# Kernel optimization log

Hardware: AMD Instinct MI355X
Metric: run time of the kernel (lower is better)

The kernel has to match this reference:

```python
import jax, jax.numpy as jnp
import numpy as np

B, K, L, H = 64, 32, 64, 256


def setup_inputs() -> dict:
    key = jax.random.key(0)
    ks = jax.random.split(key, 24)
    def rnd(i, shape, scale):
        return jax.random.normal(ks[i], shape, dtype=jnp.float32) * scale
    s = 0.05  # small init for weights to keep activations sane
    return {
        'h_ue': rnd(0, (B, K, H), 1.0),
        'h_ap': rnd(1, (B, L, H), 1.0),
        'e':    rnd(2, (B, L * K, H), 1.0),
        # msg_ap_to_ue: Linear(2H->H), Linear(H->H)
        'a2u_w1': rnd(3, (H, 2 * H), s), 'a2u_b1': rnd(4, (H,), s),
        'a2u_w2': rnd(5, (H, H), s),     'a2u_b2': rnd(6, (H,), s),
        # msg_ue_to_ap
        'u2a_w1': rnd(7, (H, 2 * H), s), 'u2a_b1': rnd(8, (H,), s),
        'u2a_w2': rnd(9, (H, H), s),     'u2a_b2': rnd(10, (H,), s),
        # GRUCell (PyTorch layout: weight_ih (3H,H), weight_hh (3H,H))
        'ue_wih': rnd(11, (3 * H, H), s), 'ue_bih': rnd(12, (3 * H,), s),
        'ue_whh': rnd(13, (3 * H, H), s), 'ue_bhh': rnd(14, (3 * H,), s),
        'ap_wih': rnd(15, (3 * H, H), s), 'ap_bih': rnd(16, (3 * H,), s),
        'ap_whh': rnd(17, (3 * H, H), s), 'ap_bhh': rnd(18, (3 * H,), s),
        # edge_update: Linear(3H->H), Linear(H->H)
        'ed_w1': rnd(19, (H, 3 * H), s), 'ed_b1': rnd(20, (H,), s),
        'ed_w2': rnd(21, (H, H), s),     'ed_b2': rnd(22, (H,), s),
    }


def _gru(x, h, wih, bih, whh, bhh):
    # PyTorch GRUCell semantics
    gi = jnp.einsum('...h,oh->...o', x, wih) + bih
    gh = jnp.einsum('...h,oh->...o', h, whh) + bhh
    i_r, i_z, i_n = jnp.split(gi, 3, axis=-1)
    h_r, h_z, h_n = jnp.split(gh, 3, axis=-1)
    r = jax.nn.sigmoid(i_r + h_r)
    z = jax.nn.sigmoid(i_z + h_z)
    n = jnp.tanh(i_n + r * h_n)
    return (1.0 - z) * n + z * h


def reference(h_ue, h_ap, e,
              a2u_w1, a2u_b1, a2u_w2, a2u_b2,
              u2a_w1, u2a_b1, u2a_w2, u2a_b2,
              ue_wih, ue_bih, ue_whh, ue_bhh,
              ap_wih, ap_bih, ap_whh, ap_bhh,
              ed_w1, ed_b1, ed_w2, ed_b2):
    Bd, Kd, Hd = h_ue.shape
    Ld = h_ap.shape[1]
    e4 = e.reshape(Bd, Ld, Kd, Hd)  # edge (b, l, k) on dense bipartite graph

    # --- AP -> UE messages: MLP(concat[h_ap_src, e]); split first linear ---
    pre = (jnp.einsum('blh,oh->blo', h_ap, a2u_w1[:, :Hd])[:, :, None, :]
           + jnp.einsum('blkh,oh->blko', e4, a2u_w1[:, Hd:]) + a2u_b1)
    msg = jnp.einsum('blkh,oh->blko', jax.nn.relu(pre), a2u_w2) + a2u_b2
    m_ue = msg.mean(axis=1)  # mean over AP neighbors -> (B,K,H)

    # --- UE -> AP messages ---
    pre = (jnp.einsum('bkh,oh->bko', h_ue, u2a_w1[:, :Hd])[:, None, :, :]
           + jnp.einsum('blkh,oh->blko', e4, u2a_w1[:, Hd:]) + u2a_b1)
    msg = jnp.einsum('blkh,oh->blko', jax.nn.relu(pre), u2a_w2) + u2a_b2
    m_ap = msg.mean(axis=2)  # mean over UE neighbors -> (B,L,H)

    # --- GRU node updates ---
    h_ue_new = _gru(m_ue, h_ue, ue_wih, ue_bih, ue_whh, ue_bhh)
    h_ap_new = _gru(m_ap, h_ap, ap_wih, ap_bih, ap_whh, ap_bhh)

    # --- edge update: MLP(concat[src=UE_new, dst=AP_new, e]) ---
    pre = (jnp.einsum('bkh,oh->bko', h_ue_new, ed_w1[:, :Hd])[:, None, :, :]
           + jnp.einsum('blh,oh->blo', h_ap_new, ed_w1[:, Hd:2 * Hd])[:, :, None, :]
           + jnp.einsum('blkh,oh->blko', e4, ed_w1[:, 2 * Hd:]) + ed_b1)
    e_new = jnp.einsum('blkh,oh->blko', jax.nn.relu(pre), ed_w2) + ed_b2

    return h_ue_new, h_ap_new, e_new.reshape(Bd, Ld * Kd, Hd)
```

## Files before the change

### kernel.cpp

```cpp
#include <hip/hip_runtime.h>

#define HH 256
#define BB 64
#define KK 32
#define LL 64
#define LGRP 8

typedef __bf16 bf16_t;
typedef __attribute__((ext_vector_type(8))) __bf16 bf16x8;
typedef __attribute__((ext_vector_type(4))) float f32x4;

__device__ __forceinline__ bf16x8 ld_a8(const float* __restrict__ p) {
  const f32x4* q = (const f32x4*)p;
  f32x4 a = q[0], b = q[1];
  bf16x8 r;
  r[0] = (__bf16)a[0]; r[1] = (__bf16)a[1]; r[2] = (__bf16)a[2]; r[3] = (__bf16)a[3];
  r[4] = (__bf16)b[0]; r[5] = (__bf16)b[1]; r[6] = (__bf16)b[2]; r[7] = (__bf16)b[3];
  return r;
}

__device__ __forceinline__ void ld_tile(const float* __restrict__ E, int tid, f32x4 r[4]) {
  const f32x4* q = (const f32x4*)(E + tid * 16);
  r[0] = q[0]; r[1] = q[1]; r[2] = q[2]; r[3] = q[3];
}
__device__ __forceinline__ void wr_tile(bf16_t* buf, int tid, const f32x4 r[4]) {
  int row = tid >> 4;
  int colb = (tid & 15) * 32;
  bf16x8 v0, v1;
  v0[0] = (__bf16)r[0][0]; v0[1] = (__bf16)r[0][1]; v0[2] = (__bf16)r[0][2]; v0[3] = (__bf16)r[0][3];
  v0[4] = (__bf16)r[1][0]; v0[5] = (__bf16)r[1][1]; v0[6] = (__bf16)r[1][2]; v0[7] = (__bf16)r[1][3];
  v1[0] = (__bf16)r[2][0]; v1[1] = (__bf16)r[2][1]; v1[2] = (__bf16)r[2][2]; v1[3] = (__bf16)r[2][3];
  v1[4] = (__bf16)r[3][0]; v1[5] = (__bf16)r[3][1]; v1[6] = (__bf16)r[3][2]; v1[7] = (__bf16)r[3][3];
  int swz = (row & 7) << 4;
  *(bf16x8*)((char*)buf + row * 512 + (colb ^ swz)) = v0;
  *(bf16x8*)((char*)buf + row * 512 + ((colb + 16) ^ swz)) = v1;
}

template<int LDB>
__device__ __forceinline__ void mm_f32A(const float* __restrict__ A,
                                        const bf16_t* __restrict__ B,
                                        f32x4 acc[2][4], int lane) {
  const int c = lane & 15, g = lane >> 4;
#pragma unroll
  for (int ks = 0; ks < 8; ++ks) {
    const int ko = ks * 32 + g * 8;
    bf16x8 a0 = ld_a8(A + c * HH + ko);
    bf16x8 a1 = ld_a8(A + (16 + c) * HH + ko);
#pragma unroll
    for (int nt = 0; nt < 4; ++nt) {
      bf16x8 bb = *(const bf16x8*)(B + (nt * 16 + c) * LDB + ko);
      acc[0][nt] = __builtin_amdgcn_mfma_f32_16x16x32_bf16(a0, bb, acc[0][nt], 0, 0, 0);
      acc[1][nt] = __builtin_amdgcn_mfma_f32_16x16x32_bf16(a1, bb, acc[1][nt], 0, 0, 0);
    }
  }
}

__global__ __launch_bounds__(256) void prep_kernel(
    const float* w0, const float* w1, const float* w2, const float* w3,
    const float* w4, const float* w5, const float* w6, const float* w7,
    const float* w8, const float* w9, bf16_t* wb) {
  int i = blockIdx.x * 256 + threadIdx.x;
  const float* s; int o; float sc = 1.f;
  if      (i < 131072)  { s = w0; o = i; }
  else if (i < 196608)  { s = w1; o = i - 131072; sc = 1.f / 64.f; }
  else if (i < 327680)  { s = w2; o = i - 196608; }
  else if (i < 393216)  { s = w3; o = i - 327680; sc = 1.f / 32.f; }
  else if (i < 589824)  { s = w4; o = i - 393216; }
  else if (i < 786432)  { s = w5; o = i - 589824; }
  else if (i < 983040)  { s = w6; o = i - 786432; }
  else if (i < 1179648) { s = w7; o = i - 983040; }
  else if (i < 1376256) { s = w8; o = i - 1179648; }
  else                  { s = w9; o = i - 1376256; }
  wb[i] = (__bf16)(s[o] * sc);
}

template<int LDW>
__global__ __launch_bounds__(256) void proj2_kernel(
    const float* __restrict__ X0, const bf16_t* __restrict__ W0,
    const float* __restrict__ b0, float* __restrict__ out0, int n0,
    const float* __restrict__ X1, const bf16_t* __restrict__ W1,
    const float* __restrict__ b1, float* __restrict__ out1) {
  const int blk = blockIdx.x;
  const float* X; const bf16_t* W; const float* bias; float* out; int row0;
  if (blk < n0) { X = X0; W = W0; bias = b0; out = out0; row0 = blk * 32; }
  else          { X = X1; W = W1; bias = b1; out = out1; row0 = (blk - n0) * 32; }
  const int tid = threadIdx.x, w = tid >> 6, lane = tid & 63;
  const int colw = w * 64, c = lane & 15, g = lane >> 4;
  f32x4 acc[2][4];
#pragma unroll
  for (int nt = 0; nt < 4; ++nt) {
    float bv = bias ? bias[colw + nt * 16 + c] : 0.f;
    f32x4 t = {bv, bv, bv, bv};
    acc[0][nt] = t; acc[1][nt] = t;
  }
  mm_f32A<LDW>(X + (size_t)row0 * HH, W + (size_t)colw * LDW, acc, lane);
#pragma unroll
  for (int m = 0; m < 2; ++m)
#pragma unroll
    for (int nt = 0; nt < 4; ++nt)
#pragma unroll
      for (int rr = 0; rr < 4; ++rr) {
        int row = row0 + m * 16 + g * 4 + rr;
        out[(size_t)row * HH + colw + nt * 16 + c] = acc[m][nt][rr];
      }
}

__global__ __launch_bounds__(512) void phaseA_kernel(
    const float* __restrict__ e, const float* __restrict__ p_ap,
    const float* __restrict__ p_ue,
    const bf16_t* __restrict__ wu1e, const bf16_t* __restrict__ wa1e,
    float* __restrict__ part, float* __restrict__ R_ap) {
  __shared__ bf16_t ebuf[2][32 * 256];
  const int blk = blockIdx.x;
  const int b = blk >> 3, lc = blk & 7;
  const int tid = threadIdx.x, w = tid >> 6, lane = tid & 63;
  const int colw = w * 32, c = lane & 15, g = lane >> 4;
  const int l0 = lc * LGRP;

  bf16x8 wU[2][8], wA[2][8];
#pragma unroll
  for (int nt = 0; nt < 2; ++nt)
#pragma unroll
    for (int ks = 0; ks < 8; ++ks) {
      size_t off = (size_t)(colw + nt * 16 + c) * 512 + ks * 32 + g * 8;
      wU[nt][ks] = *(const bf16x8*)(wu1e + off);
      wA[nt][ks] = *(const bf16x8*)(wa1e + off);
    }

  float pue[2][2][4];
#pragma unroll
  for (int m = 0; m < 2; ++m)
#pragma unroll
    for (int nt = 0; nt < 2; ++nt)
#pragma unroll
      for (int rr = 0; rr < 4; ++rr)
        pue[m][nt][rr] = p_ue[(size_t)(b * KK + m * 16 + g * 4 + rr) * HH + colw + nt * 16 + c];

  f32x4 accU[2][2];
  const f32x4 z4 = {0.f, 0.f, 0.f, 0.f};
#pragma unroll
  for (int m = 0; m < 2; ++m)
#pragma unroll
    for (int nt = 0; nt < 2; ++nt) accU[m][nt] = z4;

  f32x4 rs[4];
  ld_tile(e + (size_t)((b * LL + l0) * KK) * HH, tid, rs);
  wr_tile(ebuf[0], tid, rs);

  for (int li = 0; li < LGRP; ++li) {
    __syncthreads();
    const int l = l0 + li;
    if (li + 1 < LGRP) ld_tile(e + (size_t)((b * LL + l + 1) * KK) * HH, tid, rs);

    f32x4 aU[2][2], aA[2][2];
#pragma unroll
    for (int nt = 0; nt < 2; ++nt) {
      float pa = p_ap[(size_t)(b * LL + l) * HH + colw + nt * 16 + c];
      f32x4 t = {pa, pa, pa, pa};
      aA[0][nt] = t; aA[1][nt] = t;
#pragma unroll
      for (int rr = 0; rr < 4; ++rr) {
        aU[0][nt][rr] = pue[0][nt][rr];
        aU[1][nt][rr] = pue[1][nt][rr];
      }
    }
    const bf16_t* eb = ebuf[li & 1];
    const int swz = (c & 7) << 4;
#pragma unroll
    for (int ks = 0; ks < 8; ++ks) {
      const int kb = (ks * 32 + g * 8) * 2;
      bf16x8 a0 = *(const bf16x8*)((const char*)eb + c * 512 + (kb ^ swz));
      bf16x8 a1 = *(const bf16x8*)((const char*)eb + (16 + c) * 512 + (kb ^ swz));
#pragma unroll
      for (int nt = 0; nt < 2; ++nt) {
        aU[0][nt] = __builtin_amdgcn_mfma_f32_16x16x32_bf16(a0, wU[nt][ks], aU[0][nt], 0, 0, 0);
        aU[1][nt] = __builtin_amdgcn_mfma_f32_16x16x32_bf16(a1, wU[nt][ks], aU[1][nt], 0, 0, 0);
        aA[0][nt] = __builtin_amdgcn_mfma_f32_16x16x32_bf16(a0, wA[nt][ks], aA[0][nt], 0, 0, 0);
        aA[1][nt] = __builtin_amdgcn_mfma_f32_16x16x32_bf16(a1, wA[nt][ks], aA[1][nt], 0, 0, 0);
      }
    }
    __syncthreads();
    if (li + 1 < LGRP) wr_tile(ebuf[(li + 1) & 1], tid, rs);

#pragma unroll
    for (int nt = 0; nt < 2; ++nt) {
      float s = 0.f;
#pragma unroll
      for (int m = 0; m < 2; ++m)
#pragma unroll
        for (int rr = 0; rr < 4; ++rr) s += fmaxf(aU[m][nt][rr], 0.f);
      s += __shfl_xor(s, 16);
      s += __shfl_xor(s, 32);
      if (lane < 16)
        R_ap[(size_t)(b * LL + l) * HH + colw + nt * 16 + lane] = s;
    }
#pragma unroll
    for (int m = 0; m < 2; ++m)
#pragma unroll
      for (int nt = 0; nt < 2; ++nt)
#pragma unroll
        for (int rr = 0; rr < 4; ++rr)
          accU[m][nt][rr] += fmaxf(aA[m][nt][rr], 0.f);
  }

#pragma unroll
  for (int m = 0; m < 2; ++m)
#pragma unroll
    for (int nt = 0; nt < 2; ++nt)
#pragma unroll
      for (int rr = 0; rr < 4; ++rr) {
        int krow = m * 16 + g * 4 + rr;
        part[(size_t)((lc * BB + b) * KK + krow) * HH + colw + nt * 16 + c] = accU[m][nt][rr];
      }
}

__global__ __launch_bounds__(256) void reduce_kernel(
    const float* __restrict__ part, float* __restrict__ R_ue) {
  int i = blockIdx.x * 256 + threadIdx.x;
  float s = 0.f;
#pragma unroll
  for (int lc = 0; lc < 8; ++lc) s += part[(size_t)lc * 524288 + i];
  R_ue[i] = s;
}

__global__ __launch_bounds__(256) void gru_kernel(
    const float* __restrict__ m_ue, const float* __restrict__ h_ue,
    const bf16_t* __restrict__ wih_ue, const bf16_t* __restrict__ whh_ue,
    const float* __restrict__ ue_bih, const float* __restrict__ ue_bhh,
    float* __restrict__ hue_new,
    const float* __restrict__ m_ap, const float* __restrict__ h_ap,
    const bf16_t* __restrict__ wih_ap, const bf16_t* __restrict__ whh_ap,
    const float* __restrict__ ap_bih, const float* __restrict__ ap_bhh,
    float* __restrict__ hap_new) {
  const int blk = blockIdx.x;
  const float *x, *h, *bih, *bhh; const bf16_t *wih, *whh; float* hout; int row0;
  if (blk < 64) { x = m_ue; h = h_ue; wih = wih_ue; whh = whh_ue;
                  bih = ue_bih; bhh = ue_bhh; hout = hue_new; row0 = blk * 32; }
  else          { x = m_ap; h = h_ap; wih = wih_ap; whh = whh_ap;
                  bih = ap_bih; bhh = ap_bhh; hout = hap_new; row0 = (blk - 64) * 32; }
  const int tid = threadIdx.x, w = tid >> 6, lane = tid & 63;
  const int colw = w * 64, c = lane & 15, g = lane >> 4;
  f32x4 aR[2][4], aZ[2][4], aN[2][4], aHN[2][4];
#pragma unroll
  for (int nt = 0; nt < 4; ++nt) {
    int col = colw + nt * 16 + c;
    float vR = bih[col] + bhh[col];
    float vZ = bih[256 + col] + bhh[256 + col];
    float vN = bih[512 + col];
    float vH = bhh[512 + col];
    f32x4 tR = {vR, vR, vR, vR}, tZ = {vZ, vZ, vZ, vZ};
    f32x4 tN = {vN, vN, vN, vN}, tH = {vH, vH, vH, vH};
    aR[0][nt] = tR; aR[1][nt] = tR;
    aZ[0][nt] = tZ; aZ[1][nt] = tZ;
    aN[0][nt] = tN; aN[1][nt] = tN;
    aHN[0][nt] = tH; aHN[1][nt] = tH;
  }
  const float* X = x + (size_t)row0 * HH;
  const float* Hp = h + (size_t)row0 * HH;
  mm_f32A<256>(X,  wih + (size_t)(0   + colw) * 256, aR, lane);
  mm_f32A<256>(Hp, whh + (size_t)(0   + colw) * 256, aR, lane);
  mm_f32A<256>(X,  wih + (size_t)(256 + colw) * 256, aZ, lane);
  mm_f32A<256>(Hp, whh + (size_t)(256 + colw) * 256, aZ, lane);
  mm_f32A<256>(X,  wih + (size_t)(512 + colw) * 256, aN, lane);
  mm_f32A<256>(Hp, whh + (size_t)(512 + colw) * 256, aHN, lane);
#pragma unroll
  for (int m = 0; m < 2; ++m)
#pragma unroll
    for (int nt = 0; nt < 4; ++nt)
#pragma unroll
      for (int rr = 0; rr < 4; ++rr) {
        int row = row0 + m * 16 + g * 4 + rr;
        int col = colw + nt * 16 + c;
        float rg = 1.f / (1.f + __expf(-aR[m][nt][rr]));
        float zg = 1.f / (1.f + __expf(-aZ[m][nt][rr]));
        float t = aN[m][nt][rr] + rg * aHN[m][nt][rr];
        t = fminf(fmaxf(t, -15.f), 15.f);
        float ex = __expf(-2.f * t);
        float ng = (1.f - ex) / (1.f + ex);
        float ho = h[(size_t)row * HH + col];
        hout[(size_t)row * HH + col] = (1.f - zg) * ng + zg * ho;
      }
}

__global__ __launch_bounds__(512) void phaseC_kernel(
    const float* __restrict__ e, const float* __restrict__ q_ue,
    const float* __restrict__ q_ap,
    const bf16_t* __restrict__ wed1e, const bf16_t* __restrict__ wed2,
    const float* __restrict__ ed_b2, float* __restrict__ e_new) {
  __shared__ bf16_t ebuf[2][32 * 256];
  __shared__ bf16_t pbuf[32 * 256];
  const int blk = blockIdx.x;
  const int b = blk >> 3, lc = blk & 7;
  const int tid = threadIdx.x, w = tid >> 6, lane = tid & 63;
  const int colw = w * 32, c = lane & 15, g = lane >> 4;
  const int l0 = lc * LGRP;

  bf16x8 w1[2][8], w2[2][8];
#pragma unroll
  for (int nt = 0; nt < 2; ++nt)
#pragma unroll
    for (int ks = 0; ks < 8; ++ks) {
      w1[nt][ks] = *(const bf16x8*)(wed1e + (size_t)(colw + nt * 16 + c) * 768 + ks * 32 + g * 8);
      w2[nt][ks] = *(const bf16x8*)(wed2  + (size_t)(colw + nt * 16 + c) * 256 + ks * 32 + g * 8);
    }

  float qU[2][2][4];
#pragma unroll
  for (int m = 0; m < 2; ++m)
#pragma unroll
    for (int nt = 0; nt < 2; ++nt)
#pragma unroll
      for (int rr = 0; rr < 4; ++rr)
        qU[m][nt][rr] = q_ue[(size_t)(b * KK + m * 16 + g * 4 + rr) * HH + colw + nt * 16 + c];
  float b2v[2];
#pragma unroll
  for (int nt = 0; nt < 2; ++nt) b2v[nt] = ed_b2[colw + nt * 16 + c];

  f32x4 rs[4];
  ld_tile(e + (size_t)((b * LL + l0) * KK) * HH, tid, rs);
  wr_tile(ebuf[0], tid, rs);

  for (int li = 0; li < LGRP; ++li) {
    __syncthreads();
    const int l = l0 + li;

    f32x4 a1[2][2];
#pragma unroll
    for (int nt = 0; nt < 2; ++nt) {
      float qa = q_ap[(size_t)(b * LL + l) * HH + colw + nt * 16 + c];
#pragma unroll
      for (int rr = 0; rr < 4; ++rr) {
        a1[0][nt][rr] = qa + qU[0][nt][rr];
        a1[1][nt][rr] = qa + qU[1][nt][rr];
      }
    }
    const bf16_t* eb = ebuf[li & 1];
    const int swz = (c & 7) << 4;
#pragma unroll
    for (int ks = 0; ks < 8; ++ks) {
      const int kb = (ks * 32 + g * 8) * 2;
      bf16x8 a0 = *(const bf16x8*)((const char*)eb + c * 512 + (kb ^ swz));
      bf16x8 a1f = *(const bf16x8*)((const char*)eb + (16 + c) * 512 + (kb ^ swz));
#pragma unroll
      for (int nt = 0; nt < 2; ++nt) {
        a1[0][nt] = __builtin_amdgcn_mfma_f32_16x16x32_bf16(a0,  w1[nt][ks], a1[0][nt], 0, 0, 0);
        a1[1][nt] = __builtin_amdgcn_mfma_f32_16x16x32_bf16(a1f, w1[nt][ks], a1[1][nt], 0, 0, 0);
      }
    }
    if (li + 1 < LGRP) ld_tile(e + (size_t)((b * LL + l + 1) * KK) * HH, tid, rs);

#pragma unroll
    for (int m = 0; m < 2; ++m)
#pragma unroll
      for (int nt = 0; nt < 2; ++nt)
#pragma unroll
        for (int rr = 0; rr < 4; ++rr) {
          int row = m * 16 + g * 4 + rr;
          int col = colw + nt * 16 + c;
          float v = fmaxf(a1[m][nt][rr], 0.f);
          int off = row * 512 + ((col * 2) ^ ((row & 7) << 4));
          *(bf16_t*)((char*)pbuf + off) = (__bf16)v;
        }
    __syncthreads();

    f32x4 a2[2][2];
#pragma unroll
    for (int nt = 0; nt < 2; ++nt) {
      f32x4 t = {b2v[nt], b2v[nt], b2v[nt], b2v[nt]};
      a2[0][nt] = t; a2[1][nt] = t;
    }
#pragma unroll
    for (int ks = 0; ks < 8; ++ks) {
      const int kb = (ks * 32 + g * 8) * 2;
      bf16x8 a0 = *(const bf16x8*)((const char*)pbuf + c * 512 + (kb ^ swz));
      bf16x8 a1f = *(const bf16x8*)((const char*)pbuf + (16 + c) * 512 + (kb ^ swz));
#pragma unroll
      for (int nt = 0; nt < 2; ++nt) {
        a2[0][nt] = __builtin_amdgcn_mfma_f32_16x16x32_bf16(a0,  w2[nt][ks], a2[0][nt], 0, 0, 0);
        a2[1][nt] = __builtin_amdgcn_mfma_f32_16x16x32_bf16(a1f, w2[nt][ks], a2[1][nt], 0, 0, 0);
      }
    }
#pragma unroll
    for (int m = 0; m < 2; ++m)
#pragma unroll
      for (int nt = 0; nt < 2; ++nt)
#pragma unroll
        for (int rr = 0; rr < 4; ++rr) {
          int row = m * 16 + g * 4 + rr;
          e_new[(size_t)((b * LL + l) * KK + row) * HH + colw + nt * 16 + c] = a2[m][nt][rr];
        }
    if (li + 1 < LGRP) wr_tile(ebuf[(li + 1) & 1], tid, rs);
  }
}

extern "C" void kernel_launch(void* const* d_in, const int* in_sizes, int n_in,
                              void* d_out, int out_size, void* d_ws, size_t ws_size,
                              hipStream_t stream) {
  const float* h_ue   = (const float*)d_in[0];
  const float* h_ap   = (const float*)d_in[1];
  const float* e      = (const float*)d_in[2];
  const float* a2u_w1 = (const float*)d_in[3];
  const float* a2u_b1 = (const float*)d_in[4];
  const float* a2u_w2 = (const float*)d_in[5];
  const float* a2u_b2 = (const float*)d_in[6];
  const float* u2a_w1 = (const float*)d_in[7];
  const float* u2a_b1 = (const float*)d_in[8];
  const float* u2a_w2 = (const float*)d_in[9];
  const float* u2a_b2 = (const float*)d_in[10];
  const float* ue_wih = (const float*)d_in[11];
  const float* ue_bih = (const float*)d_in[12];
  const float* ue_whh = (const float*)d_in[13];
  const float* ue_bhh = (const float*)d_in[14];
  const float* ap_wih = (const float*)d_in[15];
  const float* ap_bih = (const float*)d_in[16];
  const float* ap_whh = (const float*)d_in[17];
  const float* ap_bhh = (const float*)d_in[18];
  const float* ed_w1  = (const float*)d_in[19];
  const float* ed_b1  = (const float*)d_in[20];
  const float* ed_w2  = (const float*)d_in[21];
  const float* ed_b2  = (const float*)d_in[22];

  bf16_t* wb      = (bf16_t*)d_ws;
  bf16_t* wa1     = wb;
  bf16_t* wa2s    = wa1 + 131072;
  bf16_t* wu1     = wa2s + 65536;
  bf16_t* wu2s    = wu1 + 131072;
  bf16_t* wih_ue  = wu2s + 65536;
  bf16_t* whh_ue  = wih_ue + 196608;
  bf16_t* wih_ap  = whh_ue + 196608;
  bf16_t* whh_ap  = wih_ap + 196608;
  bf16_t* wed1    = whh_ap + 196608;
  bf16_t* wed2    = wed1 + 196608;
  float* fbase = (float*)((char*)d_ws + 2883584);
  float* m_ue = fbase;
  float* m_ap = m_ue + 524288;
  float* p_ap = m_ap + 1048576;
  float* p_ue = p_ap + 1048576;
  float* q_ue = p_ue + 524288;
  float* q_ap = q_ue + 524288;
  float* part = q_ap + 1048576;
  float* R_ue = q_ue;
  float* R_ap = q_ap;

  float* out      = (float*)d_out;
  float* hue_new  = out;
  float* hap_new  = out + 524288;
  float* e_new    = out + 1572864;

  prep_kernel<<<5632, 256, 0, stream>>>(a2u_w1, a2u_w2, u2a_w1, u2a_w2,
                                        ue_wih, ue_whh, ap_wih, ap_whh,
                                        ed_w1, ed_w2, wb);
  proj2_kernel<512><<<192, 256, 0, stream>>>(h_ap, wa1, a2u_b1, p_ap, 128,
                                             h_ue, wu1, u2a_b1, p_ue);
  phaseA_kernel<<<512, 512, 0, stream>>>(e, p_ap, p_ue, wu1 + 256, wa1 + 256,
                                         part, R_ap);
  reduce_kernel<<<2048, 256, 0, stream>>>(part, R_ue);
  proj2_kernel<256><<<192, 256, 0, stream>>>(R_ue, wa2s, a2u_b2, m_ue, 64,
                                             R_ap, wu2s, u2a_b2, m_ap);
  gru_kernel<<<192, 256, 0, stream>>>(m_ue, h_ue, wih_ue, whh_ue, ue_bih, ue_bhh, hue_new,
                                      m_ap, h_ap, wih_ap, whh_ap, ap_bih, ap_bhh, hap_new);
  proj2_kernel<768><<<192, 256, 0, stream>>>(hue_new, wed1, ed_b1, q_ue, 64,
                                             hap_new, wed1 + 256, nullptr, q_ap);
  phaseC_kernel<<<512, 512, 0, stream>>>(e, q_ue, q_ap, wed1 + 512, wed2, ed_b2, e_new);
}
```

Measured before the change: 221.8 us.

## Fuse prep, projection, reduce and GRU kernels into three launches

Drops the weight-prep kernel and the separate projection, reduce and GRU launches. Weights are converted from fp32 to bf16 on the fly inside the consumers. The node projections are now computed redundantly inside phaseA and phaseC per block, and node_kernel fuses the partial-sum reduction, message linear and GRU, staging the message in LDS. This cuts launches from eight to three and removes intermediate buffers, at the cost of redundant per-block projection work and repeated fp32 weight loads and conversions.

Result: slower. 337.5 us (+52.1%).

```diff
diff --git a/kernel.cpp b/kernel.cpp
--- a/kernel.cpp
+++ b/kernel.cpp
@@ -16,6 +16,26 @@
   bf16x8 r;
   r[0] = (__bf16)a[0]; r[1] = (__bf16)a[1]; r[2] = (__bf16)a[2]; r[3] = (__bf16)a[3];
   r[4] = (__bf16)b[0]; r[5] = (__bf16)b[1]; r[6] = (__bf16)b[2]; r[7] = (__bf16)b[3];
+  return r;
+}
+__device__ __forceinline__ bf16x8 ld_a8s(const float* __restrict__ p, float sc) {
+  const f32x4* q = (const f32x4*)p;
+  f32x4 a = q[0], b = q[1];
+  bf16x8 r;
+  r[0] = (__bf16)(a[0]*sc); r[1] = (__bf16)(a[1]*sc); r[2] = (__bf16)(a[2]*sc); r[3] = (__bf16)(a[3]*sc);
+  r[4] = (__bf16)(b[0]*sc); r[5] = (__bf16)(b[1]*sc); r[6] = (__bf16)(b[2]*sc); r[7] = (__bf16)(b[3]*sc);
+  return r;
+}
+__device__ __forceinline__ bf16x8 ld_sum8(const float* __restrict__ p) {
+  f32x4 s0 = {0.f,0.f,0.f,0.f}, s1 = s0;
+#pragma unroll
+  for (int lc = 0; lc < 8; ++lc) {
+    const f32x4* q = (const f32x4*)(p + (size_t)lc * 524288);
+    s0 += q[0]; s1 += q[1];
+  }
+  bf16x8 r;
+  r[0] = (__bf16)s0[0]; r[1] = (__bf16)s0[1]; r[2] = (__bf16)s0[2]; r[3] = (__bf16)s0[3];
+  r[4] = (__bf16)s1[0]; r[5] = (__bf16)s1[1]; r[6] = (__bf16)s1[2]; r[7] = (__bf16)s1[3];
   return r;
 }
 
@@ -37,104 +57,146 @@
 }
 
 template<int LDB>
-__device__ __forceinline__ void mm_f32A(const float* __restrict__ A,
-                                        const bf16_t* __restrict__ B,
-                                        f32x4 acc[2][4], int lane) {
+__device__ __forceinline__ void mm_f32AB(const float* __restrict__ A,
+                                         const float* __restrict__ B,
+                                         f32x4 acc[2][4], int lane, float sc) {
   const int c = lane & 15, g = lane >> 4;
 #pragma unroll
   for (int ks = 0; ks < 8; ++ks) {
     const int ko = ks * 32 + g * 8;
-    bf16x8 a0 = ld_a8(A + c * HH + ko);
-    bf16x8 a1 = ld_a8(A + (16 + c) * HH + ko);
+    bf16x8 a0 = ld_a8(A + (size_t)c * HH + ko);
+    bf16x8 a1 = ld_a8(A + (size_t)(16 + c) * HH + ko);
 #pragma unroll
     for (int nt = 0; nt < 4; ++nt) {
-      bf16x8 bb = *(const bf16x8*)(B + (nt * 16 + c) * LDB + ko);
+      bf16x8 bb = ld_a8s(B + (size_t)(nt * 16 + c) * LDB + ko, sc);
       acc[0][nt] = __builtin_amdgcn_mfma_f32_16x16x32_bf16(a0, bb, acc[0][nt], 0, 0, 0);
       acc[1][nt] = __builtin_amdgcn_mfma_f32_16x16x32_bf16(a1, bb, acc[1][nt], 0, 0, 0);
     }
   }
 }
 
-__global__ __launch_bounds__(256) void prep_kernel(
-    const float* w0, const float* w1, const float* w2, const float* w3,
-    const float* w4, const float* w5, const float* w6, const float* w7,
-    const float* w8, const float* w9, bf16_t* wb) {
-  int i = blockIdx.x * 256 + threadIdx.x;
-  const float* s; int o; float sc = 1.f;
-  if      (i < 131072)  { s = w0; o = i; }
-  else if (i < 196608)  { s = w1; o = i - 131072; sc = 1.f / 64.f; }
-  else if (i < 327680)  { s = w2; o = i - 196608; }
-  else if (i < 393216)  { s = w3; o = i - 327680; sc = 1.f / 32.f; }
-  else if (i < 589824)  { s = w4; o = i - 393216; }
-  else if (i < 786432)  { s = w5; o = i - 589824; }
-  else if (i < 983040)  { s = w6; o = i - 786432; }
-  else if (i < 1179648) { s = w7; o = i - 983040; }
-  else if (i < 1376256) { s = w8; o = i - 1179648; }
-  else                  { s = w9; o = i - 1376256; }
-  wb[i] = (__bf16)(s[o] * sc);
-}
-
-template<int LDW>
-__global__ __launch_bounds__(256) void proj2_kernel(
-    const float* __restrict__ X0, const bf16_t* __restrict__ W0,
-    const float* __restrict__ b0, float* __restrict__ out0, int n0,
-    const float* __restrict__ X1, const bf16_t* __restrict__ W1,
-    const float* __restrict__ b1, float* __restrict__ out1) {
-  const int blk = blockIdx.x;
-  const float* X; const bf16_t* W; const float* bias; float* out; int row0;
-  if (blk < n0) { X = X0; W = W0; bias = b0; out = out0; row0 = blk * 32; }
-  else          { X = X1; W = W1; bias = b1; out = out1; row0 = (blk - n0) * 32; }
-  const int tid = threadIdx.x, w = tid >> 6, lane = tid & 63;
-  const int colw = w * 64, c = lane & 15, g = lane >> 4;
-  f32x4 acc[2][4];
-#pragma unroll
-  for (int nt = 0; nt < 4; ++nt) {
-    float bv = bias ? bias[colw + nt * 16 + c] : 0.f;
-    f32x4 t = {bv, bv, bv, bv};
-    acc[0][nt] = t; acc[1][nt] = t;
-  }
-  mm_f32A<LDW>(X + (size_t)row0 * HH, W + (size_t)colw * LDW, acc, lane);
-#pragma unroll
-  for (int m = 0; m < 2; ++m)
-#pragma unroll
-    for (int nt = 0; nt < 4; ++nt)
-#pragma unroll
-      for (int rr = 0; rr < 4; ++rr) {
-        int row = row0 + m * 16 + g * 4 + rr;
-        out[(size_t)row * HH + colw + nt * 16 + c] = acc[m][nt][rr];
-      }
+__device__ __forceinline__ void mm_partA(const float* __restrict__ P,
+                                         const float* __restrict__ B,
+                                         f32x4 acc[2][4], int lane, float sc) {
+  const int c = lane & 15, g = lane >> 4;
+#pragma unroll
+  for (int ks = 0; ks < 8; ++ks) {
+    const int ko = ks * 32 + g * 8;
+    bf16x8 a0 = ld_sum8(P + (size_t)c * HH + ko);
+    bf16x8 a1 = ld_sum8(P + (size_t)(16 + c) * HH + ko);
+#pragma unroll
+    for (int nt = 0; nt < 4; ++nt) {
+      bf16x8 bb = ld_a8s(B + (size_t)(nt * 16 + c) * HH + ko, sc);
+      acc[0][nt] = __builtin_amdgcn_mfma_f32_16x16x32_bf16(a0, bb, acc[0][nt], 0, 0, 0);
+      acc[1][nt] = __builtin_amdgcn_mfma_f32_16x16x32_bf16(a1, bb, acc[1][nt], 0, 0, 0);
+    }
+  }
+}
+
+__device__ __forceinline__ void mm_lds_f32B(const bf16_t* lds,
+                                            const float* __restrict__ B,
+                                            f32x4 acc[2][4], int lane) {
+  const int c = lane & 15, g = lane >> 4;
+  const int swz = (c & 7) << 4;
+#pragma unroll
+  for (int ks = 0; ks < 8; ++ks) {
+    const int kb = (ks * 32 + g * 8) * 2;
+    bf16x8 a0 = *(const bf16x8*)((const char*)lds + c * 512 + (kb ^ swz));
+    bf16x8 a1 = *(const bf16x8*)((const char*)lds + (16 + c) * 512 + (kb ^ swz));
+#pragma unroll
+    for (int nt = 0; nt < 4; ++nt) {
+      bf16x8 bb = ld_a8(B + (size_t)(nt * 16 + c) * HH + ks * 32 + g * 8);
+      acc[0][nt] = __builtin_amdgcn_mfma_f32_16x16x32_bf16(a0, bb, acc[0][nt], 0, 0, 0);
+      acc[1][nt] = __builtin_amdgcn_mfma_f32_16x16x32_bf16(a1, bb, acc[1][nt], 0, 0, 0);
+    }
+  }
 }
 
 __global__ __launch_bounds__(512) void phaseA_kernel(
-    const float* __restrict__ e, const float* __restrict__ p_ap,
-    const float* __restrict__ p_ue,
-    const bf16_t* __restrict__ wu1e, const bf16_t* __restrict__ wa1e,
+    const float* __restrict__ e, const float* __restrict__ h_ue,
+    const float* __restrict__ h_ap,
+    const float* __restrict__ a2u_w1, const float* __restrict__ a2u_b1,
+    const float* __restrict__ u2a_w1, const float* __restrict__ u2a_b1,
     float* __restrict__ part, float* __restrict__ R_ap) {
   __shared__ bf16_t ebuf[2][32 * 256];
+  __shared__ float pA[8 * 256];
   const int blk = blockIdx.x;
   const int b = blk >> 3, lc = blk & 7;
   const int tid = threadIdx.x, w = tid >> 6, lane = tid & 63;
   const int colw = w * 32, c = lane & 15, g = lane >> 4;
   const int l0 = lc * LGRP;
 
+  f32x4 rs[4];
+  ld_tile(e + (size_t)((b * LL + l0) * KK) * HH, tid, rs);
+
+  float pue[2][2][4];
+  {
+    f32x4 pacc[2][2];
+#pragma unroll
+    for (int nt = 0; nt < 2; ++nt) {
+      float bv = u2a_b1[colw + nt * 16 + c];
+      f32x4 t = {bv, bv, bv, bv};
+      pacc[0][nt] = t; pacc[1][nt] = t;
+    }
+#pragma unroll
+    for (int ks = 0; ks < 8; ++ks) {
+      const int ko = ks * 32 + g * 8;
+      bf16x8 a0 = ld_a8(h_ue + (size_t)(b * KK + c) * HH + ko);
+      bf16x8 a1 = ld_a8(h_ue + (size_t)(b * KK + 16 + c) * HH + ko);
+#pragma unroll
+      for (int nt = 0; nt < 2; ++nt) {
+        bf16x8 bb = ld_a8(u2a_w1 + (size_t)(colw + nt * 16 + c) * 512 + ko);
+        pacc[0][nt] = __builtin_amdgcn_mfma_f32_16x16x32_bf16(a0, bb, pacc[0][nt], 0, 0, 0);
+        pacc[1][nt] = __builtin_amdgcn_mfma_f32_16x16x32_bf16(a1, bb, pacc[1][nt], 0, 0, 0);
+      }
+    }
+#pragma unroll
+    for (int m = 0; m < 2; ++m)
+#pragma unroll
+      for (int nt = 0; nt < 2; ++nt)
+#pragma unroll
+        for (int rr = 0; rr < 4; ++rr) pue[m][nt][rr] = pacc[m][nt][rr];
+  }
+
+  {
+    f32x4 sap[2];
+#pragma unroll
+    for (int nt = 0; nt < 2; ++nt) {
+      float bv = a2u_b1[colw + nt * 16 + c];
+      f32x4 t = {bv, bv, bv, bv};
+      sap[nt] = t;
+    }
+    const float* Xap = h_ap + (size_t)(b * LL + l0) * HH;
+#pragma unroll
+    for (int ks = 0; ks < 8; ++ks) {
+      const int ko = ks * 32 + g * 8;
+      bf16x8 a = ld_a8(Xap + (size_t)(c & 7) * HH + ko);
+#pragma unroll
+      for (int nt = 0; nt < 2; ++nt) {
+        bf16x8 bb = ld_a8(a2u_w1 + (size_t)(colw + nt * 16 + c) * 512 + ko);
+        sap[nt] = __builtin_amdgcn_mfma_f32_16x16x32_bf16(a, bb, sap[nt], 0, 0, 0);
+      }
+    }
+    if (g < 2) {
+#pragma unroll
+      for (int nt = 0; nt < 2; ++nt)
+#pragma unroll
+        for (int rr = 0; rr < 4; ++rr)
+          pA[(g * 4 + rr) * 256 + colw + nt * 16 + c] = sap[nt][rr];
+    }
+  }
+
   bf16x8 wU[2][8], wA[2][8];
 #pragma unroll
   for (int nt = 0; nt < 2; ++nt)
 #pragma unroll
     for (int ks = 0; ks < 8; ++ks) {
-      size_t off = (size_t)(colw + nt * 16 + c) * 512 + ks * 32 + g * 8;
-      wU[nt][ks] = *(const bf16x8*)(wu1e + off);
-      wA[nt][ks] = *(const bf16x8*)(wa1e + off);
-    }
-
-  float pue[2][2][4];
-#pragma unroll
-  for (int m = 0; m < 2; ++m)
-#pragma unroll
-    for (int nt = 0; nt < 2; ++nt)
-#pragma unroll
-      for (int rr = 0; rr < 4; ++rr)
-        pue[m][nt][rr] = p_ue[(size_t)(b * KK + m * 16 + g * 4 + rr) * HH + colw + nt * 16 + c];
+      size_t off = (size_t)(colw + nt * 16 + c) * 512 + 256 + ks * 32 + g * 8;
+      wU[nt][ks] = ld_a8(u2a_w1 + off);
+      wA[nt][ks] = ld_a8(a2u_w1 + off);
+    }
+
+  wr_tile(ebuf[0], tid, rs);
 
   f32x4 accU[2][2];
   const f32x4 z4 = {0.f, 0.f, 0.f, 0.f};
@@ -142,10 +204,6 @@
   for (int m = 0; m < 2; ++m)
 #pragma unroll
     for (int nt = 0; nt < 2; ++nt) accU[m][nt] = z4;
-
-  f32x4 rs[4];
-  ld_tile(e + (size_t)((b * LL + l0) * KK) * HH, tid, rs);
-  wr_tile(ebuf[0], tid, rs);
 
   for (int li = 0; li < LGRP; ++li) {
     __syncthreads();
@@ -155,7 +213,7 @@
     f32x4 aU[2][2], aA[2][2];
 #pragma unroll
     for (int nt = 0; nt < 2; ++nt) {
-      float pa = p_ap[(size_t)(b * LL + l) * HH + colw + nt * 16 + c];
+      float pa = pA[li * 256 + colw + nt * 16 + c];
       f32x4 t = {pa, pa, pa, pa};
       aA[0][nt] = t; aA[1][nt] = t;
 #pragma unroll
@@ -214,32 +272,56 @@
       }
 }
 
-__global__ __launch_bounds__(256) void reduce_kernel(
-    const float* __restrict__ part, float* __restrict__ R_ue) {
-  int i = blockIdx.x * 256 + threadIdx.x;
-  float s = 0.f;
-#pragma unroll
-  for (int lc = 0; lc < 8; ++lc) s += part[(size_t)lc * 524288 + i];
-  R_ue[i] = s;
-}
-
-__global__ __launch_bounds__(256) void gru_kernel(
-    const float* __restrict__ m_ue, const float* __restrict__ h_ue,
-    const bf16_t* __restrict__ wih_ue, const bf16_t* __restrict__ whh_ue,
-    const float* __restrict__ ue_bih, const float* __restrict__ ue_bhh,
-    float* __restrict__ hue_new,
-    const float* __restrict__ m_ap, const float* __restrict__ h_ap,
-    const bf16_t* __restrict__ wih_ap, const bf16_t* __restrict__ whh_ap,
-    const float* __restrict__ ap_bih, const float* __restrict__ ap_bhh,
-    float* __restrict__ hap_new) {
+__global__ __launch_bounds__(256) void node_kernel(
+    const float* __restrict__ part, const float* __restrict__ R_ap,
+    const float* __restrict__ a2u_w2, const float* __restrict__ a2u_b2,
+    const float* __restrict__ u2a_w2, const float* __restrict__ u2a_b2,
+    const float* __restrict__ h_ue, const float* __restrict__ ue_wih,
+    const float* __restrict__ ue_bih, const float* __restrict__ ue_whh,
+    const float* __restrict__ ue_bhh,
+    const float* __restrict__ h_ap, const float* __restrict__ ap_wih,
+    const float* __restrict__ ap_bih, const float* __restrict__ ap_whh,
+    const float* __restrict__ ap_bhh,
+    float* __restrict__ hue_new, float* __restrict__ hap_new) {
+  __shared__ bf16_t mbuf[32 * 256];
   const int blk = blockIdx.x;
-  const float *x, *h, *bih, *bhh; const bf16_t *wih, *whh; float* hout; int row0;
-  if (blk < 64) { x = m_ue; h = h_ue; wih = wih_ue; whh = whh_ue;
-                  bih = ue_bih; bhh = ue_bhh; hout = hue_new; row0 = blk * 32; }
-  else          { x = m_ap; h = h_ap; wih = wih_ap; whh = whh_ap;
-                  bih = ap_bih; bhh = ap_bhh; hout = hap_new; row0 = (blk - 64) * 32; }
+  const bool ue = blk < 64;
+  const int row0 = ue ? blk * 32 : (blk - 64) * 32;
   const int tid = threadIdx.x, w = tid >> 6, lane = tid & 63;
   const int colw = w * 64, c = lane & 15, g = lane >> 4;
+  const float* W2  = ue ? a2u_w2 : u2a_w2;
+  const float* b2  = ue ? a2u_b2 : u2a_b2;
+  const float* h   = ue ? h_ue : h_ap;
+  const float* wih = ue ? ue_wih : ap_wih;
+  const float* whh = ue ? ue_whh : ap_whh;
+  const float* bih = ue ? ue_bih : ap_bih;
+  const float* bhh = ue ? ue_bhh : ap_bhh;
+  float* hout      = ue ? hue_new : hap_new;
+  const float sc   = ue ? (1.f / 64.f) : (1.f / 32.f);
+
+  f32x4 acc[2][4];
+#pragma unroll
+  for (int nt = 0; nt < 4; ++nt) {
+    float bv = b2[colw + nt * 16 + c];
+    f32x4 t = {bv, bv, bv, bv};
+    acc[0][nt] = t; acc[1][nt] = t;
+  }
+  if (ue) mm_partA(part + (size_t)row0 * HH, W2 + (size_t)colw * HH, acc, lane, sc);
+  else    mm_f32AB<HH>(R_ap + (size_t)row0 * HH, W2 + (size_t)colw * HH, acc, lane, sc);
+
+#pragma unroll
+  for (int m = 0; m < 2; ++m)
+#pragma unroll
+    for (int nt = 0; nt < 4; ++nt)
+#pragma unroll
+      for (int rr = 0; rr < 4; ++rr) {
+        int row = m * 16 + g * 4 + rr;
+        int col = colw + nt * 16 + c;
+        int off = row * 512 + ((col * 2) ^ ((row & 7) << 4));
+        *(bf16_t*)((char*)mbuf + off) = (__bf16)acc[m][nt][rr];
+      }
+  __syncthreads();
+
   f32x4 aR[2][4], aZ[2][4], aN[2][4], aHN[2][4];
 #pragma unroll
   for (int nt = 0; nt < 4; ++nt) {
@@ -255,14 +337,13 @@
     aN[0][nt] = tN; aN[1][nt] = tN;
     aHN[0][nt] = tH; aHN[1][nt] = tH;
   }
-  const float* X = x + (size_t)row0 * HH;
   const float* Hp = h + (size_t)row0 * HH;
-  mm_f32A<256>(X,  wih + (size_t)(0   + colw) * 256, aR, lane);
-  mm_f32A<256>(Hp, whh + (size_t)(0   + colw) * 256, aR, lane);
-  mm_f32A<256>(X,  wih + (size_t)(256 + colw) * 256, aZ, lane);
-  mm_f32A<256>(Hp, whh + (size_t)(256 + colw) * 256, aZ, lane);
-  mm_f32A<256>(X,  wih + (size_t)(512 + colw) * 256, aN, lane);
-  mm_f32A<256>(Hp, whh + (size_t)(512 + colw) * 256, aHN, lane);
+  mm_lds_f32B(mbuf, wih + (size_t)(0   + colw) * HH, aR, lane);
+  mm_f32AB<HH>(Hp,  whh + (size_t)(0   + colw) * HH, aR, lane, 1.f);
+  mm_lds_f32B(mbuf, wih + (size_t)(256 + colw) * HH, aZ, lane);
+  mm_f32AB<HH>(Hp,  whh + (size_t)(256 + colw) * HH, aZ, lane, 1.f);
+  mm_lds_f32B(mbuf, wih + (size_t)(512 + colw) * HH, aN, lane);
+  mm_f32AB<HH>(Hp,  whh + (size_t)(512 + colw) * HH, aHN, lane, 1.f);
 #pragma unroll
   for (int m = 0; m < 2; ++m)
 #pragma unroll
@@ -283,41 +364,88 @@
 }
 
 __global__ __launch_bounds__(512) void phaseC_kernel(
-    const float* __restrict__ e, const float* __restrict__ q_ue,
-    const float* __restrict__ q_ap,
-    const bf16_t* __restrict__ wed1e, const bf16_t* __restrict__ wed2,
-    const float* __restrict__ ed_b2, float* __restrict__ e_new) {
+    const float* __restrict__ e, const float* __restrict__ hue_new,
+    const float* __restrict__ hap_new,
+    const float* __restrict__ ed_w1, const float* __restrict__ ed_b1,
+    const float* __restrict__ ed_w2, const float* __restrict__ ed_b2,
+    float* __restrict__ e_new) {
   __shared__ bf16_t ebuf[2][32 * 256];
   __shared__ bf16_t pbuf[32 * 256];
+  __shared__ float qA[8 * 256];
   const int blk = blockIdx.x;
   const int b = blk >> 3, lc = blk & 7;
   const int tid = threadIdx.x, w = tid >> 6, lane = tid & 63;
   const int colw = w * 32, c = lane & 15, g = lane >> 4;
   const int l0 = lc * LGRP;
 
-  bf16x8 w1[2][8], w2[2][8];
-#pragma unroll
-  for (int nt = 0; nt < 2; ++nt)
-#pragma unroll
-    for (int ks = 0; ks < 8; ++ks) {
-      w1[nt][ks] = *(const bf16x8*)(wed1e + (size_t)(colw + nt * 16 + c) * 768 + ks * 32 + g * 8);
-      w2[nt][ks] = *(const bf16x8*)(wed2  + (size_t)(colw + nt * 16 + c) * 256 + ks * 32 + g * 8);
-    }
-
-  float qU[2][2][4];
-#pragma unroll
-  for (int m = 0; m < 2; ++m)
-#pragma unroll
-    for (int nt = 0; nt < 2; ++nt)
-#pragma unroll
-      for (int rr = 0; rr < 4; ++rr)
-        qU[m][nt][rr] = q_ue[(size_t)(b * KK + m * 16 + g * 4 + rr) * HH + colw + nt * 16 + c];
-  float b2v[2];
-#pragma unroll
-  for (int nt = 0; nt < 2; ++nt) b2v[nt] = ed_b2[colw + nt * 16 + c];
-
   f32x4 rs[4];
   ld_tile(e + (size_t)((b * LL + l0) * KK) * HH, tid, rs);
+
+  float qU[2][2][4];
+  {
+    f32x4 qacc[2][2];
+#pragma unroll
+    for (int nt = 0; nt < 2; ++nt) {
+      float bv = ed_b1[colw + nt * 16 + c];
+      f32x4 t = {bv, bv, bv, bv};
+      qacc[0][nt] = t; qacc[1][nt] = t;
+    }
+#pragma unroll
+    for (int ks = 0; ks < 8; ++ks) {
+      const int ko = ks * 32 + g * 8;
+      bf16x8 a0 = ld_a8(hue_new + (size_t)(b * KK + c) * HH + ko);
+      bf16x8 a1 = ld_a8(hue_new + (size_t)(b * KK + 16 + c) * HH + ko);
+#pragma unroll
+      for (int nt = 0; nt < 2; ++nt) {
+        bf16x8 bb = ld_a8(ed_w1 + (size_t)(colw + nt * 16 + c) * 768 + ko);
+        qacc[0][nt] = __builtin_amdgcn_mfma_f32_16x16x32_bf16(a0, bb, qacc[0][nt], 0, 0, 0);
+        qacc[1][nt] = __builtin_amdgcn_mfma_f32_16x16x32_bf16(a1, bb, qacc[1][nt], 0, 0, 0);
+      }
+    }
+#pragma unroll
+    for (int m = 0; m < 2; ++m)
+#pragma unroll
+      for (int nt = 0; nt < 2; ++nt)
+#pragma unroll
+        for (int rr = 0; rr < 4; ++rr) qU[m][nt][rr] = qacc[m][nt][rr];
+  }
+
+  {
+    f32x4 sap[2];
+    const f32x4 z4 = {0.f, 0.f, 0.f, 0.f};
+    sap[0] = z4; sap[1] = z4;
+    const float* Xap = hap_new + (size_t)(b * LL + l0) * HH;
+#pragma unroll
+    for (int ks = 0; ks < 8; ++ks) {
+      const int ko = ks * 32 + g * 8;
+      bf16x8 a = ld_a8(Xap + (size_t)(c & 7) * HH + ko);
+#pragma unroll
+      for (int nt = 0; nt < 2; ++nt) {
+        bf16x8 bb = ld_a8(ed_w1 + (size_t)(colw + nt * 16 + c) * 768 + 256 + ko);
+        sap[nt] = __builtin_amdgcn_mfma_f32_16x16x32_bf16(a, bb, sap[nt], 0, 0, 0);
+      }
+    }
+    if (g < 2) {
+#pragma unroll
+      for (int nt = 0; nt < 2; ++nt)
+#pragma unroll
+        for (int rr = 0; rr < 4; ++rr)
+          qA[(g * 4 + rr) * 256 + colw + nt * 16 + c] = sap[nt][rr];
+    }
+  }
+
+  bf16x8 w1[2][8], w2[2][8];
+#pragma unroll
+  for (int nt = 0; nt < 2; ++nt)
+#pragma unroll
+    for (int ks = 0; ks < 8; ++ks) {
+      w1[nt][ks] = ld_a8(ed_w1 + (size_t)(colw + nt * 16 + c) * 768 + 512 + ks * 32 + g * 8);
+      w2[nt][ks] = ld_a8(ed_w2 + (size_t)(colw + nt * 16 + c) * 256 + ks * 32 + g * 8);
+    }
+  float b2v[2];
+#pragma unroll
+  for (int nt = 0; nt < 2; ++nt) b2v[nt] = ed_b2[colw + nt * 16 + c];
+
   wr_tile(ebuf[0], tid, rs);
 
   for (int li = 0; li < LGRP; ++li) {
@@ -327,7 +455,7 @@
     f32x4 a1[2][2];
 #pragma unroll
     for (int nt = 0; nt < 2; ++nt) {
-      float qa = q_ap[(size_t)(b * LL + l) * HH + colw + nt * 16 + c];
+      float qa = qA[li * 256 + colw + nt * 16 + c];
 #pragma unroll
       for (int rr = 0; rr < 4; ++rr) {
         a1[0][nt][rr] = qa + qU[0][nt][rr];
@@ -420,46 +548,22 @@
   const float* ed_w2  = (const float*)d_in[21];
   const float* ed_b2  = (const float*)d_in[22];
 
-  bf16_t* wb      = (bf16_t*)d_ws;
-  bf16_t* wa1     = wb;
-  bf16_t* wa2s    = wa1 + 131072;
-  bf16_t* wu1     = wa2s + 65536;
-  bf16_t* wu2s    = wu1 + 131072;
-  bf16_t* wih_ue  = wu2s + 65536;
-  bf16_t* whh_ue  = wih_ue + 196608;
-  bf16_t* wih_ap  = whh_ue + 196608;
-  bf16_t* whh_ap  = wih_ap + 196608;
-  bf16_t* wed1    = whh_ap + 196608;
-  bf16_t* wed2    = wed1 + 196608;
-  float* fbase = (float*)((char*)d_ws + 2883584);
-  float* m_ue = fbase;
-  float* m_ap = m_ue + 524288;
-  float* p_ap = m_ap + 1048576;
-  float* p_ue = p_ap + 1048576;
-  float* q_ue = p_ue + 524288;
-  float* q_ap = q_ue + 524288;
-  float* part = q_ap + 1048576;
-  float* R_ue = q_ue;
-  float* R_ap = q_ap;
+  float* part = (float*)d_ws;
+  float* R_ap = part + 4194304;
 
   float* out      = (float*)d_out;
   float* hue_new  = out;
   float* hap_new  = out + 524288;
   float* e_new    = out + 1572864;
 
-  prep_kernel<<<5632, 256, 0, stream>>>(a2u_w1, a2u_w2, u2a_w1, u2a_w2,
-                                        ue_wih, ue_whh, ap_wih, ap_whh,
-                                        ed_w1, ed_w2, wb);
-  proj2_kernel<512><<<192, 256, 0, stream>>>(h_ap, wa1, a2u_b1, p_ap, 128,
-                                             h_ue, wu1, u2a_b1, p_ue);
-  phaseA_kernel<<<512, 512, 0, stream>>>(e, p_ap, p_ue, wu1 + 256, wa1 + 256,
+  phaseA_kernel<<<512, 512, 0, stream>>>(e, h_ue, h_ap,
+                                         a2u_w1, a2u_b1, u2a_w1, u2a_b1,
                                          part, R_ap);
-  reduce_kernel<<<2048, 256, 0, stream>>>(part, R_ue);
-  proj2_kernel<256><<<192, 256, 0, stream>>>(R_ue, wa2s, a2u_b2, m_ue, 64,
-                                             R_ap, wu2s, u2a_b2, m_ap);
-  gru_kernel<<<192, 256, 0, stream>>>(m_ue, h_ue, wih_ue, whh_ue, ue_bih, ue_bhh, hue_new,
-                                      m_ap, h_ap, wih_ap, whh_ap, ap_bih, ap_bhh, hap_new);
-  proj2_kernel<768><<<192, 256, 0, stream>>>(hue_new, wed1, ed_b1, q_ue, 64,
-                                             hap_new, wed1 + 256, nullptr, q_ap);
-  phaseC_kernel<<<512, 512, 0, stream>>>(e, q_ue, q_ap, wed1 + 512, wed2, ed_b2, e_new);
-}
+  node_kernel<<<192, 256, 0, stream>>>(part, R_ap,
+                                       a2u_w2, a2u_b2, u2a_w2, u2a_b2,
+                                       h_ue, ue_wih, ue_bih, ue_whh, ue_bhh,
+                                       h_ap, ap_wih, ap_bih, ap_whh, ap_bhh,
+                                       hue_new, hap_new);
+  phaseC_kernel<<<512, 512, 0, stream>>>(e, hue_new, hap_new,
+                                         ed_w1, ed_b1, ed_w2, ed_b2, e_new);
+}
```
